# Performance work log

Hardware: AMD Instinct MI355X
Metric: run time of the kernel (lower is better)

## Reference

```python
import jax, jax.numpy as jnp
import numpy as np

WS = 8
NH = 8


def setup_inputs() -> dict:
    key = jax.random.key(0)
    ks = jax.random.split(key, 5)
    B, H, W, C = 4, 256, 256, 256
    x = jax.random.normal(ks[0], (B, H * W, C), dtype=jnp.float32)
    qkv_w = jax.random.normal(ks[1], (3 * C, C), dtype=jnp.float32) * (C ** -0.5)
    proj_w = jax.random.normal(ks[2], (C, C), dtype=jnp.float32) * (C ** -0.5)
    proj_b = jnp.zeros((C,), dtype=jnp.float32)
    bias = jax.random.normal(ks[3], (NH, WS * WS, WS * WS), dtype=jnp.float32) * 0.02
    return {"x": x, "qkv_w": qkv_w, "proj_w": proj_w, "proj_b": proj_b,
            "bias": bias, "H": H, "W": W}


def reference(x, qkv_w, proj_w, proj_b, bias, H, W):
    B, L, C = x.shape
    hd = C // NH
    scale = hd ** -0.5
    pad_r = (WS - W % WS) % WS
    pad_b = (WS - H % WS) % WS
    xv = x.reshape(B, H, W, C)
    if pad_r > 0 or pad_b > 0:
        xv = jnp.pad(xv, ((0, 0), (0, pad_b), (0, pad_r), (0, 0)))
    Hp, Wp = H + pad_b, W + pad_r
    nHw, nWw = Hp // WS, Wp // WS
    # window partition -> [B*nHw*nWw, WS*WS, C]
    xw = (xv.reshape(B, nHw, WS, nWw, WS, C)
            .transpose(0, 1, 3, 2, 4, 5)
            .reshape(-1, WS * WS, C))
    # qkv: [nw, t, 3C] -> [3, nw, nh, t, hd]
    qkv = jnp.einsum('ntc,dc->ntd', xw, qkv_w)
    qkv = qkv.reshape(-1, WS * WS, 3, NH, hd).transpose(2, 0, 3, 1, 4)
    q, k, v = qkv[0], qkv[1], qkv[2]
    attn = jnp.einsum('whqd,whkd->whqk', q * scale, k) + bias[None]
    out = jnp.einsum('whqk,whkd->whqd', jax.nn.softmax(attn, axis=-1), v)
    out = out.transpose(0, 2, 1, 3).reshape(-1, WS * WS, C)
    out = jnp.einsum('ntc,dc->ntd', out, proj_w) + proj_b
    # reverse window partition
    out = (out.reshape(B, nHw, nWw, WS, WS, C)
              .transpose(0, 1, 3, 2, 4, 5)
              .reshape(B, Hp, Wp, C))
    if pad_r > 0 or pad_b > 0:
        out = out[:, :H, :W, :]
    return out.reshape(B, L, C)
```

## Files before the change

kernel.cpp:

```cpp
#include <hip/hip_runtime.h>

typedef unsigned short u16;
typedef __bf16 bf16x8 __attribute__((ext_vector_type(8)));
typedef float f32x4 __attribute__((ext_vector_type(4)));

#define MFMA(a, b, c) __builtin_amdgcn_mfma_f32_16x16x32_bf16(a, b, c, 0, 0, 0)

static __device__ __forceinline__ u16 f2bf(float f) {
  unsigned u = __float_as_uint(f);
  u = u + 0x7FFFu + ((u >> 16) & 1u);
  return (u16)(u >> 16);
}

static __device__ __forceinline__ f32x4 fzero() {
  f32x4 z; z[0] = 0.f; z[1] = 0.f; z[2] = 0.f; z[3] = 0.f; return z;
}

__global__ void cvt_w(const float* __restrict__ qw, const float* __restrict__ pw,
                      u16* __restrict__ o) {
  int i = blockIdx.x * 256 + threadIdx.x;
  float v = (i < 196608) ? qw[i] : pw[i - 196608];
  o[i] = f2bf(v);
}

#define SMEM_U16 76288

__global__ __launch_bounds__(512, 2) void swin(
    const float* __restrict__ x, const u16* __restrict__ wqkv,
    const u16* __restrict__ wproj, const float* __restrict__ pb,
    const float* __restrict__ bias, float* __restrict__ out) {

  extern __shared__ u16 smem[];

  const int tid  = threadIdx.x;
  const int wv   = tid >> 6;
  const int lane = tid & 63;
  const int l15  = lane & 15;
  const int quad = lane >> 4;

  const int w  = blockIdx.x;
  const int bb = w >> 10;
  const int wh = (w >> 5) & 31;
  const int ww = w & 31;

  u16* Xs = smem;

  {
    const float* xb = x + ((size_t)bb << 24);
    #pragma unroll
    for (int i = 0; i < 8; ++i) {
      int flat = i * 512 + tid;
      int t  = flat >> 6;
      int c4 = flat & 63;
      int row = wh * 8 + (t >> 3), col = ww * 8 + (t & 7);
      const float4 v = *(const float4*)(xb + ((size_t)(row * 256 + col) << 8) + c4 * 4);
      unsigned p0 = (unsigned)f2bf(v.x) | ((unsigned)f2bf(v.y) << 16);
      unsigned p1 = (unsigned)f2bf(v.z) | ((unsigned)f2bf(v.w) << 16);
      *(uint2*)&Xs[t * 264 + c4 * 4] = make_uint2(p0, p1);
    }
  }
  __syncthreads();

  u16* Qs = smem + 16896 + wv * 7424;
  u16* Ks = Qs + 2560;
  u16* Vt = Qs + 5120;

  {
    f32x4 acc[6][4];
    #pragma unroll
    for (int j = 0; j < 6; ++j)
      #pragma unroll
      for (int m = 0; m < 4; ++m) acc[j][m] = fzero();

    #pragma unroll
    for (int kk = 0; kk < 8; ++kk) {
      bf16x8 af[4];
      #pragma unroll
      for (int m = 0; m < 4; ++m)
        af[m] = *(const bf16x8*)&Xs[(m * 16 + l15) * 264 + kk * 32 + quad * 8];
      #pragma unroll
      for (int j = 0; j < 6; ++j) {
        int ty = j >> 1, sub = j & 1;
        int r0 = ty * 256 + wv * 32 + sub * 16;
        bf16x8 bf = *(const bf16x8*)(wqkv + (size_t)(r0 + l15) * 256 + kk * 32 + quad * 8);
        #pragma unroll
        for (int m = 0; m < 4; ++m) acc[j][m] = MFMA(af[m], bf, acc[j][m]);
      }
    }
    #pragma unroll
    for (int j = 0; j < 6; ++j) {
      int ty = j >> 1, sub = j & 1;
      int dl = sub * 16 + l15;
      #pragma unroll
      for (int m = 0; m < 4; ++m) {
        if (ty == 2) {
          unsigned p0 = (unsigned)f2bf(acc[j][m][0]) | ((unsigned)f2bf(acc[j][m][1]) << 16);
          unsigned p1 = (unsigned)f2bf(acc[j][m][2]) | ((unsigned)f2bf(acc[j][m][3]) << 16);
          *(uint2*)&Vt[dl * 72 + m * 16 + quad * 4] = make_uint2(p0, p1);
        } else {
          u16* dst = ty ? Ks : Qs;
          #pragma unroll
          for (int e = 0; e < 4; ++e)
            dst[(m * 16 + quad * 4 + e) * 40 + dl] = f2bf(acc[j][m][e]);
        }
      }
    }
  }
  __syncthreads();

  const float scale = 0.17677669529663687f;
  float sb[4][4][4];
  float rinv[4][4];
  {
    const float* bh = bias + wv * 4096;
    float bv[4][4][4];
    #pragma unroll
    for (int m = 0; m < 4; ++m)
      #pragma unroll
      for (int n = 0; n < 4; ++n)
        #pragma unroll
        for (int e = 0; e < 4; ++e)
          bv[m][n][e] = bh[(m * 16 + quad * 4 + e) * 64 + n * 16 + l15];

    f32x4 sacc[4][4];
    #pragma unroll
    for (int m = 0; m < 4; ++m)
      #pragma unroll
      for (int n = 0; n < 4; ++n) sacc[m][n] = fzero();

    bf16x8 qa[4];
    #pragma unroll
    for (int m = 0; m < 4; ++m)
      qa[m] = *(const bf16x8*)&Qs[(m * 16 + l15) * 40 + quad * 8];
    #pragma unroll
    for (int n = 0; n < 4; ++n) {
      bf16x8 kb = *(const bf16x8*)&Ks[(n * 16 + l15) * 40 + quad * 8];
      #pragma unroll
      for (int m = 0; m < 4; ++m) sacc[m][n] = MFMA(qa[m], kb, sacc[m][n]);
    }
    #pragma unroll
    for (int m = 0; m < 4; ++m)
      #pragma unroll
      for (int n = 0; n < 4; ++n)
        #pragma unroll
        for (int e = 0; e < 4; ++e)
          sb[m][n][e] = sacc[m][n][e] * scale + bv[m][n][e];
  }
  #pragma unroll
  for (int m = 0; m < 4; ++m)
    #pragma unroll
    for (int e = 0; e < 4; ++e) {
      float mx = fmaxf(fmaxf(sb[m][0][e], sb[m][1][e]), fmaxf(sb[m][2][e], sb[m][3][e]));
      #pragma unroll
      for (int d = 1; d < 16; d <<= 1) mx = fmaxf(mx, __shfl_xor(mx, d, 64));
      float sum = 0.f;
      #pragma unroll
      for (int n = 0; n < 4; ++n) {
        float p = __expf(sb[m][n][e] - mx);
        sb[m][n][e] = p; sum += p;
      }
      #pragma unroll
      for (int d = 1; d < 16; d <<= 1) sum += __shfl_xor(sum, d, 64);
      rinv[m][e] = __builtin_amdgcn_rcpf(sum);
    }
  u16* Ps = Qs;
  #pragma unroll
  for (int m = 0; m < 4; ++m)
    #pragma unroll
    for (int n = 0; n < 4; ++n)
      #pragma unroll
      for (int e = 0; e < 4; ++e)
        Ps[(m * 16 + quad * 4 + e) * 72 + n * 16 + l15] = f2bf(sb[m][n][e]);

  {
    f32x4 oacc[4][2];
    #pragma unroll
    for (int m = 0; m < 4; ++m)
      #pragma unroll
      for (int n = 0; n < 2; ++n) oacc[m][n] = fzero();
    #pragma unroll
    for (int kk = 0; kk < 2; ++kk) {
      bf16x8 pa[4];
      #pragma unroll
      for (int m = 0; m < 4; ++m)
        pa[m] = *(const bf16x8*)&Ps[(m * 16 + l15) * 72 + kk * 32 + quad * 8];
      #pragma unroll
      for (int n = 0; n < 2; ++n) {
        bf16x8 vb = *(const bf16x8*)&Vt[(n * 16 + l15) * 72 + kk * 32 + quad * 8];
        #pragma unroll
        for (int m = 0; m < 4; ++m) oacc[m][n] = MFMA(pa[m], vb, oacc[m][n]);
      }
    }
    u16* Os = Xs;
    #pragma unroll
    for (int m = 0; m < 4; ++m)
      #pragma unroll
      for (int n = 0; n < 2; ++n)
        #pragma unroll
        for (int e = 0; e < 4; ++e)
          Os[(m * 16 + quad * 4 + e) * 264 + wv * 32 + n * 16 + l15] =
              f2bf(oacc[m][n][e] * rinv[m][e]);
  }
  __syncthreads();

  {
    u16* Os = Xs;
    f32x4 pacc[4][2];
    #pragma unroll
    for (int m = 0; m < 4; ++m)
      #pragma unroll
      for (int n = 0; n < 2; ++n) pacc[m][n] = fzero();
    const int n0 = wv * 32;
    #pragma unroll
    for (int kk = 0; kk < 8; ++kk) {
      bf16x8 af[4];
      #pragma unroll
      for (int m = 0; m < 4; ++m)
        af[m] = *(const bf16x8*)&Os[(m * 16 + l15) * 264 + kk * 32 + quad * 8];
      #pragma unroll
      for (int n = 0; n < 2; ++n) {
        bf16x8 bf = *(const bf16x8*)(wproj + (size_t)(n0 + n * 16 + l15) * 256 + kk * 32 + quad * 8);
        #pragma unroll
        for (int m = 0; m < 4; ++m) pacc[m][n] = MFMA(af[m], bf, pacc[m][n]);
      }
    }
    float* ob = out + ((size_t)bb << 24);
    #pragma unroll
    for (int n = 0; n < 2; ++n) {
      float bvv = pb[n0 + n * 16 + l15];
      #pragma unroll
      for (int m = 0; m < 4; ++m)
        #pragma unroll
        for (int e = 0; e < 4; ++e) {
          int t = m * 16 + quad * 4 + e;
          int row = wh * 8 + (t >> 3), col = ww * 8 + (t & 7);
          ob[((size_t)(row * 256 + col) << 8) + n0 + n * 16 + l15] = pacc[m][n][e] + bvv;
        }
    }
  }
}

extern "C" void kernel_launch(void* const* d_in, const int* in_sizes, int n_in,
                              void* d_out, int out_size, void* d_ws, size_t ws_size,
                              hipStream_t stream) {
  const float* x  = (const float*)d_in[0];
  const float* qw = (const float*)d_in[1];
  const float* pw = (const float*)d_in[2];
  const float* pb = (const float*)d_in[3];
  const float* bs = (const float*)d_in[4];
  u16* wbf = (u16*)d_ws;

  static bool lds_opt_in = false;
  if (!lds_opt_in) {
    hipFuncSetAttribute((const void*)swin,
                        hipFuncAttributeMaxDynamicSharedMemorySize, SMEM_U16 * 2);
    lds_opt_in = true;
  }

  cvt_w<<<1024, 256, 0, stream>>>(qw, pw, wbf);
  swin<<<4096, 512, SMEM_U16 * 2, stream>>>(x, wbf, wbf + 196608, pb, bs, (float*)d_out);
}
```

Measured before the change: 793.8 us.

## Persistent 1024-thread blocks looping over windows with prefetched input and register-resident P

Turns the kernel into a persistent design: 256 blocks of 1024 threads each process 16 windows in sequence. The input tile for the next window is prefetched into registers during attention, and the relative-position bias is loaded once per block. Attention is split across two waves per head, computing S^T so softmax reduces with two cross-lane shuffles, and P stays in registers (redistributed by shuffles) instead of going through LDS. Packed bf16 conversion instructions are also used. In exchange, the grid is small (256 blocks, possibly under one per CU), a 1024-thread block with launch_bounds(1024,4) limits registers per thread, and each window adds extra barriers.

```diff
diff --git a/kernel.cpp b/kernel.cpp
--- a/kernel.cpp
+++ b/kernel.cpp
@@ -3,6 +3,7 @@
 typedef unsigned short u16;
 typedef __bf16 bf16x8 __attribute__((ext_vector_type(8)));
 typedef float f32x4 __attribute__((ext_vector_type(4)));
+typedef unsigned uint4v __attribute__((ext_vector_type(4)));
 
 #define MFMA(a, b, c) __builtin_amdgcn_mfma_f32_16x16x32_bf16(a, b, c, 0, 0, 0)
 
@@ -10,6 +11,12 @@
   unsigned u = __float_as_uint(f);
   u = u + 0x7FFFu + ((u >> 16) & 1u);
   return (u16)(u >> 16);
+}
+
+static __device__ __forceinline__ unsigned pk2(float lo, float hi) {
+  unsigned r;
+  asm("v_cvt_pk_bf16_f32 %0, %1, %2" : "=v"(r) : "v"(lo), "v"(hi));
+  return r;
 }
 
 static __device__ __forceinline__ f32x4 fzero() {
@@ -23,9 +30,22 @@
   o[i] = f2bf(v);
 }
 
+static __device__ __forceinline__ void load_x(const float* __restrict__ x, int w,
+                                              int tid, float4 xr[4]) {
+  const int bb = w >> 10, wh = (w >> 5) & 31, ww = w & 31;
+  const float* xb = x + ((size_t)bb << 24);
+  #pragma unroll
+  for (int i = 0; i < 4; ++i) {
+    int flat = i * 1024 + tid;
+    int t = flat >> 6, c4 = flat & 63;
+    int row = wh * 8 + (t >> 3), col = ww * 8 + (t & 7);
+    xr[i] = *(const float4*)(xb + ((size_t)(row * 256 + col) << 8) + c4 * 4);
+  }
+}
+
 #define SMEM_U16 76288
 
-__global__ __launch_bounds__(512, 2) void swin(
+__global__ __launch_bounds__(1024, 4) void swin(
     const float* __restrict__ x, const u16* __restrict__ wqkv,
     const u16* __restrict__ wproj, const float* __restrict__ pb,
     const float* __restrict__ bias, float* __restrict__ out) {
@@ -37,204 +57,223 @@
   const int lane = tid & 63;
   const int l15  = lane & 15;
   const int quad = lane >> 4;
-
-  const int w  = blockIdx.x;
-  const int bb = w >> 10;
-  const int wh = (w >> 5) & 31;
-  const int ww = w & 31;
+  const int h    = wv >> 1;
+  const int hf   = wv & 1;
 
   u16* Xs = smem;
-
+  u16* Qh = smem + 16896 + h * 7424;
+  u16* Kh = Qh + 2560;
+  u16* Vh = Qh + 5120;
+
+  float bv[4][2][4];
   {
-    const float* xb = x + ((size_t)bb << 24);
+    const float* bh = bias + h * 4096 + (hf * 32 + l15) * 64 + quad * 4;
     #pragma unroll
-    for (int i = 0; i < 8; ++i) {
-      int flat = i * 512 + tid;
-      int t  = flat >> 6;
-      int c4 = flat & 63;
-      int row = wh * 8 + (t >> 3), col = ww * 8 + (t & 7);
-      const float4 v = *(const float4*)(xb + ((size_t)(row * 256 + col) << 8) + c4 * 4);
-      unsigned p0 = (unsigned)f2bf(v.x) | ((unsigned)f2bf(v.y) << 16);
-      unsigned p1 = (unsigned)f2bf(v.z) | ((unsigned)f2bf(v.w) << 16);
+    for (int n = 0; n < 2; ++n)
+      #pragma unroll
+      for (int mk = 0; mk < 4; ++mk)
+        #pragma unroll
+        for (int e = 0; e < 4; ++e)
+          bv[mk][n][e] = bh[n * 1024 + mk * 16 + e];
+  }
+  const float pbv = pb[wv * 16 + l15];
+  const float scale = 0.17677669529663687f;
+
+  const u16* wq0 = wqkv + (size_t)(wv * 48 + l15) * 256 + quad * 8;
+  const u16* wp0 = wproj + (size_t)(wv * 16 + l15) * 256 + quad * 8;
+
+  const int wbase = blockIdx.x << 4;
+  float4 xr[4];
+  load_x(x, wbase, tid, xr);
+
+  for (int wi = 0; wi < 16; ++wi) {
+    const int w  = wbase + wi;
+    const int bb = w >> 10, wh = (w >> 5) & 31, ww = w & 31;
+
+    __syncthreads();
+    #pragma unroll
+    for (int i = 0; i < 4; ++i) {
+      int flat = i * 1024 + tid;
+      int t = flat >> 6, c4 = flat & 63;
+      unsigned p0 = (unsigned)f2bf(xr[i].x) | ((unsigned)f2bf(xr[i].y) << 16);
+      unsigned p1 = (unsigned)f2bf(xr[i].z) | ((unsigned)f2bf(xr[i].w) << 16);
       *(uint2*)&Xs[t * 264 + c4 * 4] = make_uint2(p0, p1);
     }
-  }
-  __syncthreads();
-
-  u16* Qs = smem + 16896 + wv * 7424;
-  u16* Ks = Qs + 2560;
-  u16* Vt = Qs + 5120;
-
-  {
-    f32x4 acc[6][4];
-    #pragma unroll
-    for (int j = 0; j < 6; ++j)
-      #pragma unroll
-      for (int m = 0; m < 4; ++m) acc[j][m] = fzero();
-
-    #pragma unroll
-    for (int kk = 0; kk < 8; ++kk) {
-      bf16x8 af[4];
-      #pragma unroll
-      for (int m = 0; m < 4; ++m)
-        af[m] = *(const bf16x8*)&Xs[(m * 16 + l15) * 264 + kk * 32 + quad * 8];
-      #pragma unroll
-      for (int j = 0; j < 6; ++j) {
-        int ty = j >> 1, sub = j & 1;
-        int r0 = ty * 256 + wv * 32 + sub * 16;
-        bf16x8 bf = *(const bf16x8*)(wqkv + (size_t)(r0 + l15) * 256 + kk * 32 + quad * 8);
-        #pragma unroll
-        for (int m = 0; m < 4; ++m) acc[j][m] = MFMA(af[m], bf, acc[j][m]);
-      }
-    }
-    #pragma unroll
-    for (int j = 0; j < 6; ++j) {
-      int ty = j >> 1, sub = j & 1;
-      int dl = sub * 16 + l15;
-      #pragma unroll
-      for (int m = 0; m < 4; ++m) {
+    __syncthreads();
+
+    {
+      f32x4 acc[3][4];
+      #pragma unroll
+      for (int t = 0; t < 3; ++t)
+        #pragma unroll
+        for (int m = 0; m < 4; ++m) acc[t][m] = fzero();
+
+      #pragma unroll
+      for (int kk = 0; kk < 8; ++kk) {
+        bf16x8 af[4];
+        #pragma unroll
+        for (int m = 0; m < 4; ++m)
+          af[m] = *(const bf16x8*)&Xs[(m * 16 + l15) * 264 + kk * 32 + quad * 8];
+        #pragma unroll
+        for (int t = 0; t < 3; ++t) {
+          bf16x8 bf = *(const bf16x8*)(wq0 + (size_t)t * 4096 + kk * 32);
+          #pragma unroll
+          for (int m = 0; m < 4; ++m) acc[t][m] = MFMA(af[m], bf, acc[t][m]);
+        }
+      }
+      #pragma unroll
+      for (int t = 0; t < 3; ++t) {
+        int grow = wv * 48 + t * 16;
+        int ty = grow >> 8, hd = (grow >> 5) & 7, sub = (grow >> 4) & 1;
+        u16* hb = smem + 16896 + hd * 7424;
+        int dl = sub * 16 + l15;
         if (ty == 2) {
-          unsigned p0 = (unsigned)f2bf(acc[j][m][0]) | ((unsigned)f2bf(acc[j][m][1]) << 16);
-          unsigned p1 = (unsigned)f2bf(acc[j][m][2]) | ((unsigned)f2bf(acc[j][m][3]) << 16);
-          *(uint2*)&Vt[dl * 72 + m * 16 + quad * 4] = make_uint2(p0, p1);
+          u16* vt = hb + 5120;
+          #pragma unroll
+          for (int m = 0; m < 4; ++m) {
+            unsigned p0 = pk2(acc[t][m][0], acc[t][m][1]);
+            unsigned p1 = pk2(acc[t][m][2], acc[t][m][3]);
+            *(uint2*)&vt[dl * 72 + m * 16 + quad * 4] = make_uint2(p0, p1);
+          }
         } else {
-          u16* dst = ty ? Ks : Qs;
+          u16* dst = hb + (ty ? 2560 : 0);
+          #pragma unroll
+          for (int m = 0; m < 4; ++m)
+            #pragma unroll
+            for (int e = 0; e < 4; ++e)
+              dst[(m * 16 + quad * 4 + e) * 40 + dl] = f2bf(acc[t][m][e]);
+        }
+      }
+    }
+    __syncthreads();
+
+    if (wi < 15) load_x(x, w + 1, tid, xr);
+
+    unsigned pks[4][2][2];
+    {
+      f32x4 sa[4][2];
+      #pragma unroll
+      for (int mk = 0; mk < 4; ++mk)
+        #pragma unroll
+        for (int n = 0; n < 2; ++n) sa[mk][n] = fzero();
+
+      bf16x8 ka[4], qb[2];
+      #pragma unroll
+      for (int mk = 0; mk < 4; ++mk)
+        ka[mk] = *(const bf16x8*)&Kh[(mk * 16 + l15) * 40 + quad * 8];
+      #pragma unroll
+      for (int n = 0; n < 2; ++n)
+        qb[n] = *(const bf16x8*)&Qh[(hf * 32 + n * 16 + l15) * 40 + quad * 8];
+      #pragma unroll
+      for (int mk = 0; mk < 4; ++mk)
+        #pragma unroll
+        for (int n = 0; n < 2; ++n) sa[mk][n] = MFMA(ka[mk], qb[n], sa[mk][n]);
+
+      float p[4][2][4];
+      #pragma unroll
+      for (int mk = 0; mk < 4; ++mk)
+        #pragma unroll
+        for (int n = 0; n < 2; ++n)
           #pragma unroll
           for (int e = 0; e < 4; ++e)
-            dst[(m * 16 + quad * 4 + e) * 40 + dl] = f2bf(acc[j][m][e]);
-        }
-      }
-    }
-  }
-  __syncthreads();
-
-  const float scale = 0.17677669529663687f;
-  float sb[4][4][4];
-  float rinv[4][4];
-  {
-    const float* bh = bias + wv * 4096;
-    float bv[4][4][4];
-    #pragma unroll
-    for (int m = 0; m < 4; ++m)
-      #pragma unroll
-      for (int n = 0; n < 4; ++n)
-        #pragma unroll
-        for (int e = 0; e < 4; ++e)
-          bv[m][n][e] = bh[(m * 16 + quad * 4 + e) * 64 + n * 16 + l15];
-
-    f32x4 sacc[4][4];
-    #pragma unroll
-    for (int m = 0; m < 4; ++m)
-      #pragma unroll
-      for (int n = 0; n < 4; ++n) sacc[m][n] = fzero();
-
-    bf16x8 qa[4];
-    #pragma unroll
-    for (int m = 0; m < 4; ++m)
-      qa[m] = *(const bf16x8*)&Qs[(m * 16 + l15) * 40 + quad * 8];
-    #pragma unroll
-    for (int n = 0; n < 4; ++n) {
-      bf16x8 kb = *(const bf16x8*)&Ks[(n * 16 + l15) * 40 + quad * 8];
-      #pragma unroll
-      for (int m = 0; m < 4; ++m) sacc[m][n] = MFMA(qa[m], kb, sacc[m][n]);
-    }
-    #pragma unroll
-    for (int m = 0; m < 4; ++m)
-      #pragma unroll
-      for (int n = 0; n < 4; ++n)
-        #pragma unroll
-        for (int e = 0; e < 4; ++e)
-          sb[m][n][e] = sacc[m][n][e] * scale + bv[m][n][e];
-  }
-  #pragma unroll
-  for (int m = 0; m < 4; ++m)
-    #pragma unroll
-    for (int e = 0; e < 4; ++e) {
-      float mx = fmaxf(fmaxf(sb[m][0][e], sb[m][1][e]), fmaxf(sb[m][2][e], sb[m][3][e]));
-      #pragma unroll
-      for (int d = 1; d < 16; d <<= 1) mx = fmaxf(mx, __shfl_xor(mx, d, 64));
-      float sum = 0.f;
-      #pragma unroll
-      for (int n = 0; n < 4; ++n) {
-        float p = __expf(sb[m][n][e] - mx);
-        sb[m][n][e] = p; sum += p;
-      }
-      #pragma unroll
-      for (int d = 1; d < 16; d <<= 1) sum += __shfl_xor(sum, d, 64);
-      rinv[m][e] = __builtin_amdgcn_rcpf(sum);
-    }
-  u16* Ps = Qs;
-  #pragma unroll
-  for (int m = 0; m < 4; ++m)
-    #pragma unroll
-    for (int n = 0; n < 4; ++n)
-      #pragma unroll
-      for (int e = 0; e < 4; ++e)
-        Ps[(m * 16 + quad * 4 + e) * 72 + n * 16 + l15] = f2bf(sb[m][n][e]);
-
-  {
-    f32x4 oacc[4][2];
-    #pragma unroll
-    for (int m = 0; m < 4; ++m)
-      #pragma unroll
-      for (int n = 0; n < 2; ++n) oacc[m][n] = fzero();
-    #pragma unroll
-    for (int kk = 0; kk < 2; ++kk) {
-      bf16x8 pa[4];
-      #pragma unroll
-      for (int m = 0; m < 4; ++m)
-        pa[m] = *(const bf16x8*)&Ps[(m * 16 + l15) * 72 + kk * 32 + quad * 8];
+            p[mk][n][e] = sa[mk][n][e] * scale + bv[mk][n][e];
+
       #pragma unroll
       for (int n = 0; n < 2; ++n) {
-        bf16x8 vb = *(const bf16x8*)&Vt[(n * 16 + l15) * 72 + kk * 32 + quad * 8];
-        #pragma unroll
-        for (int m = 0; m < 4; ++m) oacc[m][n] = MFMA(pa[m], vb, oacc[m][n]);
-      }
-    }
-    u16* Os = Xs;
-    #pragma unroll
-    for (int m = 0; m < 4; ++m)
+        float mx = p[0][n][0];
+        #pragma unroll
+        for (int mk = 0; mk < 4; ++mk)
+          #pragma unroll
+          for (int e = 0; e < 4; ++e) mx = fmaxf(mx, p[mk][n][e]);
+        mx = fmaxf(mx, __shfl_xor(mx, 16, 64));
+        mx = fmaxf(mx, __shfl_xor(mx, 32, 64));
+        float sum = 0.f;
+        #pragma unroll
+        for (int mk = 0; mk < 4; ++mk)
+          #pragma unroll
+          for (int e = 0; e < 4; ++e) {
+            float pe = __expf(p[mk][n][e] - mx);
+            p[mk][n][e] = pe; sum += pe;
+          }
+        sum += __shfl_xor(sum, 16, 64);
+        sum += __shfl_xor(sum, 32, 64);
+        float ri = __builtin_amdgcn_rcpf(sum);
+        #pragma unroll
+        for (int mk = 0; mk < 4; ++mk) {
+          pks[mk][n][0] = pk2(p[mk][n][0] * ri, p[mk][n][1] * ri);
+          pks[mk][n][1] = pk2(p[mk][n][2] * ri, p[mk][n][3] * ri);
+        }
+      }
+    }
+
+    {
+      const int srcA = l15 + ((quad & 1) << 5);
+      const bool hiMk = (quad & 2) != 0;
+      f32x4 oacc[2][2];
       #pragma unroll
       for (int n = 0; n < 2; ++n)
         #pragma unroll
-        for (int e = 0; e < 4; ++e)
-          Os[(m * 16 + quad * 4 + e) * 264 + wv * 32 + n * 16 + l15] =
-              f2bf(oacc[m][n][e] * rinv[m][e]);
-  }
-  __syncthreads();
-
-  {
-    u16* Os = Xs;
-    f32x4 pacc[4][2];
-    #pragma unroll
-    for (int m = 0; m < 4; ++m)
-      #pragma unroll
-      for (int n = 0; n < 2; ++n) pacc[m][n] = fzero();
-    const int n0 = wv * 32;
-    #pragma unroll
-    for (int kk = 0; kk < 8; ++kk) {
-      bf16x8 af[4];
-      #pragma unroll
-      for (int m = 0; m < 4; ++m)
-        af[m] = *(const bf16x8*)&Os[(m * 16 + l15) * 264 + kk * 32 + quad * 8];
-      #pragma unroll
-      for (int n = 0; n < 2; ++n) {
-        bf16x8 bf = *(const bf16x8*)(wproj + (size_t)(n0 + n * 16 + l15) * 256 + kk * 32 + quad * 8);
-        #pragma unroll
-        for (int m = 0; m < 4; ++m) pacc[m][n] = MFMA(af[m], bf, pacc[m][n]);
-      }
-    }
-    float* ob = out + ((size_t)bb << 24);
-    #pragma unroll
-    for (int n = 0; n < 2; ++n) {
-      float bvv = pb[n0 + n * 16 + l15];
+        for (int dt = 0; dt < 2; ++dt) oacc[n][dt] = fzero();
+
+      #pragma unroll
+      for (int kp = 0; kp < 2; ++kp) {
+        bf16x8 vvb[2];
+        #pragma unroll
+        for (int dt = 0; dt < 2; ++dt)
+          vvb[dt] = *(const bf16x8*)&Vh[(dt * 16 + l15) * 72 + kp * 32 + quad * 8];
+        #pragma unroll
+        for (int n = 0; n < 2; ++n) {
+          unsigned a0 = __shfl(pks[2 * kp][n][0], srcA, 64);
+          unsigned a1 = __shfl(pks[2 * kp][n][1], srcA, 64);
+          unsigned a2 = __shfl(pks[2 * kp][n][0], srcA + 16, 64);
+          unsigned a3 = __shfl(pks[2 * kp][n][1], srcA + 16, 64);
+          unsigned b0 = __shfl(pks[2 * kp + 1][n][0], srcA, 64);
+          unsigned b1 = __shfl(pks[2 * kp + 1][n][1], srcA, 64);
+          unsigned b2 = __shfl(pks[2 * kp + 1][n][0], srcA + 16, 64);
+          unsigned b3 = __shfl(pks[2 * kp + 1][n][1], srcA + 16, 64);
+          uint4v u;
+          u[0] = hiMk ? b0 : a0;
+          u[1] = hiMk ? b1 : a1;
+          u[2] = hiMk ? b2 : a2;
+          u[3] = hiMk ? b3 : a3;
+          bf16x8 pa = __builtin_bit_cast(bf16x8, u);
+          #pragma unroll
+          for (int dt = 0; dt < 2; ++dt) oacc[n][dt] = MFMA(pa, vvb[dt], oacc[n][dt]);
+        }
+      }
+      #pragma unroll
+      for (int n = 0; n < 2; ++n)
+        #pragma unroll
+        for (int dt = 0; dt < 2; ++dt)
+          #pragma unroll
+          for (int e = 0; e < 4; ++e)
+            Xs[(hf * 32 + n * 16 + quad * 4 + e) * 264 + h * 32 + dt * 16 + l15] =
+                f2bf(oacc[n][dt][e]);
+    }
+    __syncthreads();
+
+    {
+      f32x4 pacc[4];
+      #pragma unroll
+      for (int m = 0; m < 4; ++m) pacc[m] = fzero();
+      #pragma unroll
+      for (int kk = 0; kk < 8; ++kk) {
+        bf16x8 af[4];
+        #pragma unroll
+        for (int m = 0; m < 4; ++m)
+          af[m] = *(const bf16x8*)&Xs[(m * 16 + l15) * 264 + kk * 32 + quad * 8];
+        bf16x8 bf = *(const bf16x8*)(wp0 + kk * 32);
+        #pragma unroll
+        for (int m = 0; m < 4; ++m) pacc[m] = MFMA(af[m], bf, pacc[m]);
+      }
+      float* ob = out + ((size_t)bb << 24);
       #pragma unroll
       for (int m = 0; m < 4; ++m)
         #pragma unroll
         for (int e = 0; e < 4; ++e) {
           int t = m * 16 + quad * 4 + e;
           int row = wh * 8 + (t >> 3), col = ww * 8 + (t & 7);
-          ob[((size_t)(row * 256 + col) << 8) + n0 + n * 16 + l15] = pacc[m][n][e] + bvv;
+          ob[((size_t)(row * 256 + col) << 8) + wv * 16 + l15] = pacc[m][e] + pbv;
         }
     }
   }
@@ -258,5 +297,5 @@
   }
 
   cvt_w<<<1024, 256, 0, stream>>>(qw, pw, wbf);
-  swin<<<4096, 512, SMEM_U16 * 2, stream>>>(x, wbf, wbf + 196608, pb, bs, (float*)d_out);
-}
+  swin<<<256, 1024, SMEM_U16 * 2, stream>>>(x, wbf, wbf + 196608, pb, bs, (float*)d_out);
+}
```

New measurement: 826.9 us. 4.2% more time.
